# Kernel tuning notes

Measured on AMD Instinct MI355X. Metric: run time of the kernel, lower is better.

The kernel has to match this reference:

```python
import jax, jax.numpy as jnp
import numpy as np

B, N, D, H, K, R = 128, 2048, 256, 16, 32, 16
LEAKY_SLOPE = 0.01


def setup_inputs() -> dict:
    key = jax.random.key(0)
    ks = jax.random.split(key, 8)
    s = 0.05
    inp = jax.random.normal(ks[0], (B * N, D), dtype=jnp.float32)
    batch_ids = jnp.repeat(jnp.arange(B, dtype=jnp.int32), N)  # equal-size graphs
    Wk = jax.random.normal(ks[1], (K, D), dtype=jnp.float32) * s
    Wq0 = jax.random.normal(ks[2], (H * K, D), dtype=jnp.float32) * s
    Wq1 = jax.random.normal(ks[3], (H * K, D), dtype=jnp.float32) * s
    We = jax.random.normal(ks[4], (R, D), dtype=jnp.float32) * s
    Wout = jax.random.normal(ks[5], (D, H * R), dtype=jnp.float32) * s
    bout = jax.random.normal(ks[6], (D,), dtype=jnp.float32) * s
    return {"inp": inp, "batch_ids": batch_ids, "Wk": Wk, "Wq0": Wq0,
            "Wq1": Wq1, "We": We, "Wout": Wout, "bout": bout}


def reference(inp, batch_ids, Wk, Wq0, Wq1, We, Wout, bout):
    b = int(jnp.max(batch_ids)) + 1  # number of graphs (static at trace time)
    d = inp.shape[-1]
    # global max pool per graph (torch_geometric global_max_pool)
    pooled = jax.ops.segment_max(inp, batch_ids, num_segments=b)  # [B, D]
    x = inp.reshape(b, -1, d)                                     # [B, N, D]
    keys = jnp.einsum('bnd,kd->bnk', x, Wk)                       # [B, N, K]

    def head_embed(Wq):
        q = (pooled @ Wq.T).reshape(b, H, K)                      # [B, H, K]
        logits = jnp.einsum('bhk,bnk->bhn', q, keys)              # [B, H, N]
        att = jax.nn.softmax(logits, axis=-1)
        feat = jnp.einsum('bhn,bnd->bhd', att, x)                 # [B, H, D]
        return jnp.einsum('bhd,rd->bhr', feat, We)                # [B, H, R]

    dx = (head_embed(Wq0) - head_embed(Wq1)).reshape(b, -1)       # [B, H*R]
    out = dx @ Wout.T + bout
    return jnp.where(out >= 0, out, LEAKY_SLOPE * out)            # LeakyReLU
```

## Files before the change

### kernel.cpp

```cpp
#include <hip/hip_runtime.h>
#include <math.h>

#define B_ 128
#define N_ 2048
#define D_ 256
#define NHEADS 32

#define POOLED_OFF 0
#define P_OFF      32768
#define LOG_OFF    1081344
#define FEATP_OFF  9469952

__device__ __forceinline__ void atomic_max_f32(float* addr, float v) {
    if (v >= 0.0f) {
        atomicMax((int*)addr, __float_as_int(v + 0.0f));
    } else {
        atomicMin((unsigned int*)addr, __float_as_uint(v));
    }
}

__global__ __launch_bounds__(256) void k_init(float* __restrict__ pooled) {
    pooled[blockIdx.x * 256 + threadIdx.x] = -INFINITY;
}

__global__ __launch_bounds__(256) void k_pool(const float* __restrict__ inp,
                                              float* __restrict__ pooled) {
    int b = blockIdx.x >> 4;
    int chunk = blockIdx.x & 15;
    int d = threadIdx.x;
    const float* p = inp + ((size_t)(b * N_ + chunk * 128)) * D_ + d;
    float m = -INFINITY;
#pragma unroll 8
    for (int i = 0; i < 128; ++i) m = fmaxf(m, p[(size_t)i * D_]);
    atomic_max_f32(pooled + b * D_ + d, m);
}

__global__ __launch_bounds__(256) void k_qp(const float* __restrict__ pooled,
                                            const float* __restrict__ Wq0,
                                            const float* __restrict__ Wq1,
                                            const float* __restrict__ Wk,
                                            float* __restrict__ P) {
    __shared__ float pl[D_];
    __shared__ float ql[1024];
    int b = blockIdx.x, t = threadIdx.x;
    pl[t] = pooled[b * D_ + t];
    __syncthreads();
    for (int rep = 0; rep < 4; ++rep) {
        int idx = rep * 256 + t;
        const float* Wq = (idx < 512) ? Wq0 : Wq1;
        int row = idx & 511;
        const float4* wr = (const float4*)(Wq + (size_t)row * D_);
        float acc = 0.0f;
        for (int dq = 0; dq < 64; ++dq) {
            float4 w = wr[dq];
            const float* pp = &pl[dq * 4];
            acc += w.x * pp[0] + w.y * pp[1] + w.z * pp[2] + w.w * pp[3];
        }
        ql[idx] = acc;
    }
    __syncthreads();
    float wk[32];
#pragma unroll
    for (int k = 0; k < 32; ++k) wk[k] = Wk[k * D_ + t];
    for (int j = 0; j < NHEADS; ++j) {
        const float* q = &ql[(j >> 4) * 512 + (j & 15) * 32];
        float acc = 0.0f;
#pragma unroll
        for (int k = 0; k < 32; ++k) acc = fmaf(q[k], wk[k], acc);
        P[((size_t)b * NHEADS + j) * D_ + t] = acc;
    }
}

__global__ __launch_bounds__(256) void k_logits(const float* __restrict__ inp,
                                                const float* __restrict__ P,
                                                float* __restrict__ logits) {
    __shared__ float xs[512 * 20];
    __shared__ float ps[NHEADS * 20];
    int b = blockIdx.x >> 2, nt = blockIdx.x & 3;
    int n0 = nt * 512;
    int t = threadIdx.x;
    int jg = t & 3, ng = t >> 2;
    float acc[8][8] = {};
    const float* xbase = inp + ((size_t)(b * N_ + n0)) * D_;
    const float* pbase = P + (size_t)b * NHEADS * D_;
    for (int c = 0; c < 16; ++c) {
        int d0 = c * 16;
        {
            int q = t & 3, nrow = t >> 2;
            for (int k = 0; k < 8; ++k) {
                int n = nrow + k * 64;
                float4 v = *(const float4*)(xbase + (size_t)n * D_ + d0 + q * 4);
                *(float4*)&xs[n * 20 + q * 4] = v;
            }
            if (t < 128) {
                int j = t >> 2;
                float4 v = *(const float4*)(pbase + (size_t)j * D_ + d0 + q * 4);
                *(float4*)&ps[j * 20 + q * 4] = v;
            }
        }
        __syncthreads();
#pragma unroll
        for (int dd = 0; dd < 16; dd += 4) {
            float4 xa[8], pa[8];
#pragma unroll
            for (int k = 0; k < 8; ++k)
                xa[k] = *(const float4*)&xs[(ng + 64 * k) * 20 + dd];
#pragma unroll
            for (int jj = 0; jj < 8; ++jj)
                pa[jj] = *(const float4*)&ps[(jg + 4 * jj) * 20 + dd];
#pragma unroll
            for (int jj = 0; jj < 8; ++jj)
#pragma unroll
                for (int k = 0; k < 8; ++k)
                    acc[jj][k] += xa[k].x * pa[jj].x + xa[k].y * pa[jj].y +
                                  xa[k].z * pa[jj].z + xa[k].w * pa[jj].w;
        }
        __syncthreads();
    }
#pragma unroll
    for (int jj = 0; jj < 8; ++jj) {
        int j = jg + 4 * jj;
        float* lb = logits + ((size_t)b * NHEADS + j) * N_ + n0 + ng;
#pragma unroll
        for (int k = 0; k < 8; ++k) lb[64 * k] = acc[jj][k];
    }
}

__global__ __launch_bounds__(256) void k_softmax(float* __restrict__ logits) {
    float* row = logits + (size_t)blockIdx.x * N_;
    int t = threadIdx.x;
    float4 v0 = *(const float4*)(row + t * 8);
    float4 v1 = *(const float4*)(row + t * 8 + 4);
    float m = fmaxf(fmaxf(fmaxf(v0.x, v0.y), fmaxf(v0.z, v0.w)),
                    fmaxf(fmaxf(v1.x, v1.y), fmaxf(v1.z, v1.w)));
#pragma unroll
    for (int off = 32; off; off >>= 1) m = fmaxf(m, __shfl_xor(m, off, 64));
    __shared__ float smax[4];
    __shared__ float ssum[4];
    int wid = t >> 6;
    if ((t & 63) == 0) smax[wid] = m;
    __syncthreads();
    m = fmaxf(fmaxf(smax[0], smax[1]), fmaxf(smax[2], smax[3]));
    float w[8];
    w[0] = __expf(v0.x - m); w[1] = __expf(v0.y - m);
    w[2] = __expf(v0.z - m); w[3] = __expf(v0.w - m);
    w[4] = __expf(v1.x - m); w[5] = __expf(v1.y - m);
    w[6] = __expf(v1.z - m); w[7] = __expf(v1.w - m);
    float s = 0.0f;
#pragma unroll
    for (int i = 0; i < 8; ++i) s += w[i];
#pragma unroll
    for (int off = 32; off; off >>= 1) s += __shfl_xor(s, off, 64);
    if ((t & 63) == 0) ssum[wid] = s;
    __syncthreads();
    s = ssum[0] + ssum[1] + ssum[2] + ssum[3];
    float inv = 1.0f / s;
    float4 o0 = {w[0] * inv, w[1] * inv, w[2] * inv, w[3] * inv};
    float4 o1 = {w[4] * inv, w[5] * inv, w[6] * inv, w[7] * inv};
    *(float4*)(row + t * 8) = o0;
    *(float4*)(row + t * 8 + 4) = o1;
}

__global__ __launch_bounds__(256) void k_feat(const float* __restrict__ inp,
                                              const float* __restrict__ att,
                                              float* __restrict__ featp) {
    __shared__ float xs[32 * 256];
    __shared__ float as_[32 * 36];
    int b = blockIdx.x >> 2, ns = blockIdx.x & 3;
    int n0 = ns * 512;
    int t = threadIdx.x;
    int dg = t & 31, jg = t >> 5;
    float4 accA[4] = {};
    float4 accB[4] = {};
    const float* xb = inp + ((size_t)(b * N_ + n0)) * D_;
    const float* ab = att + (size_t)b * NHEADS * N_ + n0;
    for (int c = 0; c < 16; ++c) {
        {
            int q = t & 63, row = t >> 6;
            for (int k = 0; k < 8; ++k) {
                int n = row + k * 4;
                *(float4*)&xs[n * 256 + q * 4] =
                    *(const float4*)(xb + (size_t)(c * 32 + n) * D_ + q * 4);
            }
            int j = t >> 3, qq = t & 7;
            *(float4*)&as_[j * 36 + qq * 4] =
                *(const float4*)(ab + (size_t)j * N_ + c * 32 + qq * 4);
        }
        __syncthreads();
#pragma unroll
        for (int nn = 0; nn < 32; nn += 4) {
            float4 aa[4];
#pragma unroll
            for (int jj = 0; jj < 4; ++jj)
                aa[jj] = *(const float4*)&as_[(jg * 4 + jj) * 36 + nn];
#pragma unroll
            for (int i4 = 0; i4 < 4; ++i4) {
                int n = nn + i4;
                float4 xA = *(const float4*)&xs[n * 256 + dg * 4];
                float4 xB = *(const float4*)&xs[n * 256 + 128 + dg * 4];
#pragma unroll
                for (int jj = 0; jj < 4; ++jj) {
                    float a = (i4 == 0) ? aa[jj].x : (i4 == 1) ? aa[jj].y
                            : (i4 == 2) ? aa[jj].z : aa[jj].w;
                    accA[jj].x = fmaf(a, xA.x, accA[jj].x);
                    accA[jj].y = fmaf(a, xA.y, accA[jj].y);
                    accA[jj].z = fmaf(a, xA.z, accA[jj].z);
                    accA[jj].w = fmaf(a, xA.w, accA[jj].w);
                    accB[jj].x = fmaf(a, xB.x, accB[jj].x);
                    accB[jj].y = fmaf(a, xB.y, accB[jj].y);
                    accB[jj].z = fmaf(a, xB.z, accB[jj].z);
                    accB[jj].w = fmaf(a, xB.w, accB[jj].w);
                }
            }
        }
        __syncthreads();
    }
    float* fb = featp + ((size_t)ns * B_ + b) * NHEADS * D_;
#pragma unroll
    for (int jj = 0; jj < 4; ++jj) {
        int j = jg * 4 + jj;
        *(float4*)(fb + (size_t)j * D_ + dg * 4) = accA[jj];
        *(float4*)(fb + (size_t)j * D_ + 128 + dg * 4) = accB[jj];
    }
}

__global__ __launch_bounds__(256) void k_out(const float* __restrict__ featp,
                                             const float* __restrict__ We,
                                             const float* __restrict__ Wout,
                                             const float* __restrict__ bout,
                                             float* __restrict__ out) {
    __shared__ float f[NHEADS * 257];
    __shared__ float bhrs[512];
    __shared__ float dxs[256];
    int b = blockIdx.x, t = threadIdx.x;
    for (int j = 0; j < NHEADS; ++j) {
        float s = 0.0f;
#pragma unroll
        for (int ns = 0; ns < 4; ++ns)
            s += featp[(((size_t)ns * B_ + b) * NHEADS + j) * D_ + t];
        f[j * 257 + t] = s;
    }
    __syncthreads();
    for (int rep = 0; rep < 2; ++rep) {
        int idx = rep * 256 + t;
        int j = idx >> 4, r = idx & 15;
        const float* w = We + (size_t)r * D_;
        const float* ff = &f[j * 257];
        float acc = 0.0f;
        for (int d = 0; d < D_; ++d) acc = fmaf(ff[d], w[d], acc);
        bhrs[idx] = acc;
    }
    __syncthreads();
    {
        int h = t >> 4, r = t & 15;
        dxs[t] = bhrs[h * 16 + r] - bhrs[(16 + h) * 16 + r];
    }
    __syncthreads();
    float acc = bout[t];
    const float* wrow = Wout + (size_t)t * 256;
    for (int c = 0; c < 256; ++c) acc = fmaf(dxs[c], wrow[c], acc);
    out[(size_t)b * D_ + t] = acc >= 0.0f ? acc : 0.01f * acc;
}

extern "C" void kernel_launch(void* const* d_in, const int* in_sizes, int n_in,
                              void* d_out, int out_size, void* d_ws, size_t ws_size,
                              hipStream_t stream) {
    const float* inp  = (const float*)d_in[0];
    const float* Wk   = (const float*)d_in[2];
    const float* Wq0  = (const float*)d_in[3];
    const float* Wq1  = (const float*)d_in[4];
    const float* We   = (const float*)d_in[5];
    const float* Wout = (const float*)d_in[6];
    const float* bout = (const float*)d_in[7];
    float* out = (float*)d_out;
    float* ws  = (float*)d_ws;
    float* pooled = ws + POOLED_OFF;
    float* P      = ws + P_OFF;
    float* logits = ws + LOG_OFF;
    float* featp  = ws + FEATP_OFF;

    k_init<<<dim3(128), dim3(256), 0, stream>>>(pooled);
    k_pool<<<dim3(2048), dim3(256), 0, stream>>>(inp, pooled);
    k_qp<<<dim3(128), dim3(256), 0, stream>>>(pooled, Wq0, Wq1, Wk, P);
    k_logits<<<dim3(512), dim3(256), 0, stream>>>(inp, P, logits);
    k_softmax<<<dim3(4096), dim3(256), 0, stream>>>(logits);
    k_feat<<<dim3(512), dim3(256), 0, stream>>>(inp, logits, featp);
    k_out<<<dim3(128), dim3(256), 0, stream>>>(featp, We, Wout, bout, out);
}
```

Measured before the change: 679.2 us.

## Fuse softmax into logits kernel with split max/sum and bf16 exp storage

Removes the separate softmax kernel. The logits kernel now computes per-tile row maxima, writes exp(logit - tile max) as bf16, and stores a (max, sum) pair per tile. The feature kernel rescales each tile by exp(tile max - global max), and the output kernel applies the global 1/L normalization. This cuts global traffic on the 32xN attention matrix (one bf16 write and read instead of fp32 write, read-modify-write, and read) at the cost of bf16 rounding of the attention weights. The pool kernel is also vectorized to float4 with a shared-memory reduction.

```diff
diff --git a/kernel.cpp b/kernel.cpp
--- a/kernel.cpp
+++ b/kernel.cpp
@@ -8,8 +8,9 @@
 
 #define POOLED_OFF 0
 #define P_OFF      32768
-#define LOG_OFF    1081344
-#define FEATP_OFF  9469952
+#define E_OFF      1081344
+#define ML_OFF     5275648
+#define FEATP_OFF  5308416
 
 __device__ __forceinline__ void atomic_max_f32(float* addr, float v) {
     if (v >= 0.0f) {
@@ -19,6 +20,15 @@
     }
 }
 
+__device__ __forceinline__ unsigned short f2bf(float f) {
+    unsigned u = __float_as_uint(f);
+    u += 0x7fff + ((u >> 16) & 1);
+    return (unsigned short)(u >> 16);
+}
+__device__ __forceinline__ float bf2f(unsigned short h) {
+    return __uint_as_float(((unsigned)h) << 16);
+}
+
 __global__ __launch_bounds__(256) void k_init(float* __restrict__ pooled) {
     pooled[blockIdx.x * 256 + threadIdx.x] = -INFINITY;
 }
@@ -26,13 +36,26 @@
 __global__ __launch_bounds__(256) void k_pool(const float* __restrict__ inp,
                                               float* __restrict__ pooled) {
     int b = blockIdx.x >> 4;
-    int chunk = blockIdx.x & 15;
-    int d = threadIdx.x;
-    const float* p = inp + ((size_t)(b * N_ + chunk * 128)) * D_ + d;
-    float m = -INFINITY;
+    int ch = blockIdx.x & 15;
+    int t = threadIdx.x;
+    int sub = t >> 6;
+    int dq = (t & 63) * 4;
+    const float* p = inp + ((size_t)(b * N_ + ch * 128 + sub)) * D_ + dq;
+    float4 m = {-INFINITY, -INFINITY, -INFINITY, -INFINITY};
 #pragma unroll 8
-    for (int i = 0; i < 128; ++i) m = fmaxf(m, p[(size_t)i * D_]);
-    atomic_max_f32(pooled + b * D_ + d, m);
+    for (int i = 0; i < 32; ++i) {
+        float4 v = *(const float4*)(p + (size_t)i * 4 * D_);
+        m.x = fmaxf(m.x, v.x); m.y = fmaxf(m.y, v.y);
+        m.z = fmaxf(m.z, v.z); m.w = fmaxf(m.w, v.w);
+    }
+    __shared__ float sm[4 * 256];
+    sm[sub * 256 + dq + 0] = m.x;
+    sm[sub * 256 + dq + 1] = m.y;
+    sm[sub * 256 + dq + 2] = m.z;
+    sm[sub * 256 + dq + 3] = m.w;
+    __syncthreads();
+    float v = fmaxf(fmaxf(sm[t], sm[256 + t]), fmaxf(sm[512 + t], sm[768 + t]));
+    atomic_max_f32(pooled + b * D_ + t, v);
 }
 
 __global__ __launch_bounds__(256) void k_qp(const float* __restrict__ pooled,
@@ -71,9 +94,10 @@
     }
 }
 
-__global__ __launch_bounds__(256) void k_logits(const float* __restrict__ inp,
-                                                const float* __restrict__ P,
-                                                float* __restrict__ logits) {
+__global__ __launch_bounds__(256) void k_logits_e(const float* __restrict__ inp,
+                                                  const float* __restrict__ P,
+                                                  unsigned short* __restrict__ E,
+                                                  float* __restrict__ ml) {
     __shared__ float xs[512 * 20];
     __shared__ float ps[NHEADS * 20];
     int b = blockIdx.x >> 2, nt = blockIdx.x & 3;
@@ -117,63 +141,88 @@
         }
         __syncthreads();
     }
+    float* red  = xs;
+    float* red2 = xs + 2048;
+    float* mrow = xs + 2048 + 256;
+    int jr = t >> 3, pr = t & 7;
+#pragma unroll
+    for (int jj = 0; jj < 8; ++jj) {
+        float lm = acc[jj][0];
+#pragma unroll
+        for (int k = 1; k < 8; ++k) lm = fmaxf(lm, acc[jj][k]);
+        red[(jg + 4 * jj) * 64 + ng] = lm;
+    }
+    __syncthreads();
+    {
+        float v = red[jr * 64 + pr * 8];
+#pragma unroll
+        for (int i = 1; i < 8; ++i) v = fmaxf(v, red[jr * 64 + pr * 8 + i]);
+        red2[jr * 8 + pr] = v;
+    }
+    __syncthreads();
+    if (t < 32) {
+        float v = red2[t * 8];
+#pragma unroll
+        for (int i = 1; i < 8; ++i) v = fmaxf(v, red2[t * 8 + i]);
+        mrow[t] = v;
+    }
+    __syncthreads();
 #pragma unroll
     for (int jj = 0; jj < 8; ++jj) {
         int j = jg + 4 * jj;
-        float* lb = logits + ((size_t)b * NHEADS + j) * N_ + n0 + ng;
-#pragma unroll
-        for (int k = 0; k < 8; ++k) lb[64 * k] = acc[jj][k];
-    }
-}
-
-__global__ __launch_bounds__(256) void k_softmax(float* __restrict__ logits) {
-    float* row = logits + (size_t)blockIdx.x * N_;
-    int t = threadIdx.x;
-    float4 v0 = *(const float4*)(row + t * 8);
-    float4 v1 = *(const float4*)(row + t * 8 + 4);
-    float m = fmaxf(fmaxf(fmaxf(v0.x, v0.y), fmaxf(v0.z, v0.w)),
-                    fmaxf(fmaxf(v1.x, v1.y), fmaxf(v1.z, v1.w)));
-#pragma unroll
-    for (int off = 32; off; off >>= 1) m = fmaxf(m, __shfl_xor(m, off, 64));
-    __shared__ float smax[4];
-    __shared__ float ssum[4];
-    int wid = t >> 6;
-    if ((t & 63) == 0) smax[wid] = m;
-    __syncthreads();
-    m = fmaxf(fmaxf(smax[0], smax[1]), fmaxf(smax[2], smax[3]));
-    float w[8];
-    w[0] = __expf(v0.x - m); w[1] = __expf(v0.y - m);
-    w[2] = __expf(v0.z - m); w[3] = __expf(v0.w - m);
-    w[4] = __expf(v1.x - m); w[5] = __expf(v1.y - m);
-    w[6] = __expf(v1.z - m); w[7] = __expf(v1.w - m);
-    float s = 0.0f;
-#pragma unroll
-    for (int i = 0; i < 8; ++i) s += w[i];
-#pragma unroll
-    for (int off = 32; off; off >>= 1) s += __shfl_xor(s, off, 64);
-    if ((t & 63) == 0) ssum[wid] = s;
-    __syncthreads();
-    s = ssum[0] + ssum[1] + ssum[2] + ssum[3];
-    float inv = 1.0f / s;
-    float4 o0 = {w[0] * inv, w[1] * inv, w[2] * inv, w[3] * inv};
-    float4 o1 = {w[4] * inv, w[5] * inv, w[6] * inv, w[7] * inv};
-    *(float4*)(row + t * 8) = o0;
-    *(float4*)(row + t * 8 + 4) = o1;
+        float m = mrow[j];
+        unsigned short* Eb = E + ((size_t)b * NHEADS + j) * N_ + n0 + ng;
+        float s = 0.0f;
+#pragma unroll
+        for (int k = 0; k < 8; ++k) {
+            float e = __expf(acc[jj][k] - m);
+            s += e;
+            Eb[64 * k] = f2bf(e);
+        }
+        red[j * 64 + ng] = s;
+    }
+    __syncthreads();
+    {
+        float v = 0.0f;
+#pragma unroll
+        for (int i = 0; i < 8; ++i) v += red[jr * 64 + pr * 8 + i];
+        red2[jr * 8 + pr] = v;
+    }
+    __syncthreads();
+    if (t < 32) {
+        float v = 0.0f;
+#pragma unroll
+        for (int i = 0; i < 8; ++i) v += red2[t * 8 + i];
+        float* mlp = ml + (((size_t)b * NHEADS + t) * 4 + nt) * 2;
+        mlp[0] = mrow[t];
+        mlp[1] = v;
+    }
 }
 
 __global__ __launch_bounds__(256) void k_feat(const float* __restrict__ inp,
-                                              const float* __restrict__ att,
+                                              const unsigned short* __restrict__ E,
+                                              const float* __restrict__ ml,
                                               float* __restrict__ featp) {
     __shared__ float xs[32 * 256];
     __shared__ float as_[32 * 36];
+    __shared__ float wcs[32];
     int b = blockIdx.x >> 2, ns = blockIdx.x & 3;
     int n0 = ns * 512;
     int t = threadIdx.x;
     int dg = t & 31, jg = t >> 5;
+    if (t < 32) {
+        const float* mlb = ml + ((size_t)b * NHEADS + t) * 8;
+        float M = fmaxf(fmaxf(mlb[0], mlb[2]), fmaxf(mlb[4], mlb[6]));
+        wcs[t] = __expf(mlb[ns * 2] - M);
+    }
     float4 accA[4] = {};
     float4 accB[4] = {};
     const float* xb = inp + ((size_t)(b * N_ + n0)) * D_;
-    const float* ab = att + (size_t)b * NHEADS * N_ + n0;
+    const unsigned short* eb0 = E + (size_t)b * NHEADS * N_ + n0;
+    __syncthreads();
+    int js = t >> 3, qq = t & 7;
+    float wj = wcs[js];
+    const unsigned short* ebj = eb0 + (size_t)js * N_ + qq * 4;
     for (int c = 0; c < 16; ++c) {
         {
             int q = t & 63, row = t >> 6;
@@ -182,9 +231,10 @@
                 *(float4*)&xs[n * 256 + q * 4] =
                     *(const float4*)(xb + (size_t)(c * 32 + n) * D_ + q * 4);
             }
-            int j = t >> 3, qq = t & 7;
-            *(float4*)&as_[j * 36 + qq * 4] =
-                *(const float4*)(ab + (size_t)j * N_ + c * 32 + qq * 4);
+            ushort4 ev = *(const ushort4*)(ebj + c * 32);
+            float4 av = {bf2f(ev.x) * wj, bf2f(ev.y) * wj,
+                         bf2f(ev.z) * wj, bf2f(ev.w) * wj};
+            *(float4*)&as_[js * 36 + qq * 4] = av;
         }
         __syncthreads();
 #pragma unroll
@@ -225,6 +275,7 @@
 }
 
 __global__ __launch_bounds__(256) void k_out(const float* __restrict__ featp,
+                                             const float* __restrict__ ml,
                                              const float* __restrict__ We,
                                              const float* __restrict__ Wout,
                                              const float* __restrict__ bout,
@@ -232,13 +283,22 @@
     __shared__ float f[NHEADS * 257];
     __shared__ float bhrs[512];
     __shared__ float dxs[256];
+    __shared__ float linv[NHEADS];
     int b = blockIdx.x, t = threadIdx.x;
+    if (t < 32) {
+        const float* mlb = ml + ((size_t)b * NHEADS + t) * 8;
+        float M = fmaxf(fmaxf(mlb[0], mlb[2]), fmaxf(mlb[4], mlb[6]));
+        float L = __expf(mlb[0] - M) * mlb[1] + __expf(mlb[2] - M) * mlb[3] +
+                  __expf(mlb[4] - M) * mlb[5] + __expf(mlb[6] - M) * mlb[7];
+        linv[t] = 1.0f / L;
+    }
+    __syncthreads();
     for (int j = 0; j < NHEADS; ++j) {
         float s = 0.0f;
 #pragma unroll
         for (int ns = 0; ns < 4; ++ns)
             s += featp[(((size_t)ns * B_ + b) * NHEADS + j) * D_ + t];
-        f[j * 257 + t] = s;
+        f[j * 257 + t] = s * linv[j];
     }
     __syncthreads();
     for (int rep = 0; rep < 2; ++rep) {
@@ -276,14 +336,14 @@
     float* ws  = (float*)d_ws;
     float* pooled = ws + POOLED_OFF;
     float* P      = ws + P_OFF;
-    float* logits = ws + LOG_OFF;
+    unsigned short* E = (unsigned short*)(ws + E_OFF);
+    float* ml     = ws + ML_OFF;
     float* featp  = ws + FEATP_OFF;
 
     k_init<<<dim3(128), dim3(256), 0, stream>>>(pooled);
     k_pool<<<dim3(2048), dim3(256), 0, stream>>>(inp, pooled);
     k_qp<<<dim3(128), dim3(256), 0, stream>>>(pooled, Wq0, Wq1, Wk, P);
-    k_logits<<<dim3(512), dim3(256), 0, stream>>>(inp, P, logits);
-    k_softmax<<<dim3(4096), dim3(256), 0, stream>>>(logits);
-    k_feat<<<dim3(512), dim3(256), 0, stream>>>(inp, logits, featp);
-    k_out<<<dim3(128), dim3(256), 0, stream>>>(featp, We, Wout, bout, out);
-}
+    k_logits_e<<<dim3(512), dim3(256), 0, stream>>>(inp, P, E, ml);
+    k_feat<<<dim3(512), dim3(256), 0, stream>>>(inp, E, ml, featp);
+    k_out<<<dim3(128), dim3(256), 0, stream>>>(featp, ml, We, Wout, bout, out);
+}
```

Result: faster. 664.4 us (-2.2%).
